# Performance work log

Hardware: AMD Instinct MI355X
Metric: run time of the kernel (lower is better)

Reference implementation:

```python
import jax, jax.numpy as jnp
import numpy as np

N, M, D_IN, D_TXT, D_OUT, H = 4096, 1024, 512, 512, 512, 8
DH = D_OUT // H


def positional_encoding(n, dim):
    # Matches PositionalEncoding: freq = exp((arange(dim//2)/dim)*ln(10000)),
    # x = pos/freq -> [L, dim//2], interleave (sin, cos) pairs -> [L, dim].
    pos = jnp.arange(n, dtype=jnp.float32)
    freq = jnp.exp((jnp.arange(dim // 2, dtype=jnp.float32) / dim) * jnp.log(jnp.float32(10000.0)))
    x = pos[:, None] / freq  # [L, dim//2]
    pe = jnp.stack((jnp.sin(x), jnp.cos(x)), axis=-1)  # [L, dim//2, 2]
    return pe.reshape(n, dim)


def setup_inputs() -> dict:
    key = jax.random.key(0)
    k1, k2, k3, k4, k5, k6 = jax.random.split(key, 6)
    s = 0.02
    return {
        "video_features": jax.random.normal(k1, (N, D_IN), dtype=jnp.float32),
        "text_features": jax.random.normal(k2, (M, D_TXT), dtype=jnp.float32),
        "Wq": jax.random.normal(k3, (H, D_IN, DH), dtype=jnp.float32) * s,
        "Wk": jax.random.normal(k4, (H, D_TXT, DH), dtype=jnp.float32) * s,
        "Wv": jax.random.normal(k5, (H, D_TXT, DH), dtype=jnp.float32) * s,
        "Wout": jax.random.normal(k6, (D_OUT, D_IN), dtype=jnp.float32) * s,
    }


def reference(video_features, text_features, Wq, Wk, Wv, Wout):
    # Batched over heads instead of the original per-head Python loop (same math).
    Q = jnp.einsum('nd,hde->hne', video_features, Wq)   # [H, N, DH]
    K = jnp.einsum('md,hde->hme', text_features, Wk)    # [H, M, DH]
    V = jnp.einsum('md,hde->hme', text_features, Wv)    # [H, M, DH]
    energies = jnp.einsum('hne,hme->hnm', Q, K)         # no scaling in original
    att = jax.nn.softmax(energies, axis=-1)             # dropout omitted (eval mode)
    y = jnp.einsum('hnm,hme->hne', att, V)              # [H, N, DH]
    y = jnp.transpose(y, (1, 0, 2)).reshape(video_features.shape[0], -1)  # concat heads
    y = y @ Wout                                        # [N, D_IN]
    y = y + positional_encoding(y.shape[0], y.shape[1])
    return y
```

## Files before the change

kernel.cpp:

```cpp
#include <hip/hip_runtime.h>
#include <hip/hip_bf16.h>
#include <math.h>

#define N_TOK 4096
#define M_TOK 1024
#define DMODEL 512
#define NHEAD 8
#define DHEAD 64
#define LOG2E 1.44269504f

typedef __attribute__((ext_vector_type(8))) short short8;
typedef __attribute__((ext_vector_type(4))) float f32x4;
typedef __attribute__((ext_vector_type(4))) float float4v;

static __device__ __forceinline__ short f2bf(float f) {
    union { float f; unsigned u; } v; v.f = f;
    unsigned r = v.u + 0x7fffu + ((v.u >> 16) & 1u);
    return (short)(r >> 16);
}

__global__ __launch_bounds__(256) void pack_kernel(
        const float* __restrict__ xv, const float* __restrict__ xt,
        const float* __restrict__ wq, const float* __restrict__ wk,
        const float* __restrict__ wv, const float* __restrict__ wo,
        short* __restrict__ xvb, short* __restrict__ xtb,
        short* __restrict__ wqb, short* __restrict__ wkb,
        short* __restrict__ wvb, short* __restrict__ wob) {
    int bid = blockIdx.x;
    int t = threadIdx.x;
    if (bid < 256) {
        __shared__ float lds[64][65];
        const float* src;
        short* dst;
        int srstride;
        int dr0, dc0;
        if (bid < 192) {
            int mat = bid >> 6;
            int hb = bid & 63;
            int h = hb >> 3, dt = hb & 7;
            const float* W = (mat == 0) ? wq : (mat == 1) ? wk : wv;
            src = W + (size_t)h * (DMODEL * DHEAD) + (size_t)(dt * 64) * DHEAD;
            srstride = DHEAD;
            dst = (mat == 0) ? wqb : (mat == 1) ? wkb : wvb;
            dr0 = h * 64;
            dc0 = dt * 64;
        } else {
            int b = bid - 192;
            int rt = b >> 3, ct = b & 7;
            src = wo + (size_t)(rt * 64) * DMODEL + ct * 64;
            srstride = DMODEL;
            dst = wob;
            dr0 = ct * 64;
            dc0 = rt * 64;
        }
        {
            int r = t >> 2, c0 = (t & 3) * 16;
            const float* s = src + (size_t)r * srstride + c0;
            #pragma unroll
            for (int j = 0; j < 4; j++) {
                float4v v = *(const float4v*)(s + j * 4);
                lds[r][c0 + j * 4 + 0] = v[0];
                lds[r][c0 + j * 4 + 1] = v[1];
                lds[r][c0 + j * 4 + 2] = v[2];
                lds[r][c0 + j * 4 + 3] = v[3];
            }
        }
        __syncthreads();
        {
            int outr = t >> 2, c0 = (t & 3) * 16;
            short8 o0, o1;
            #pragma unroll
            for (int j = 0; j < 8; j++) {
                o0[j] = f2bf(lds[c0 + j][outr]);
                o1[j] = f2bf(lds[c0 + 8 + j][outr]);
            }
            short* d = dst + (size_t)(dr0 + outr) * DMODEL + dc0 + c0;
            *(short8*)d = o0;
            *(short8*)(d + 8) = o1;
        }
        return;
    }
    int idx = (bid - 256) * 256 + t;
    int stride = (gridDim.x - 256) * 256;
    const int CXV = N_TOK * DMODEL / 8;
    const int CXT = M_TOK * DMODEL / 8;
    for (int c = idx; c < CXV; c += stride) {
        float4v f0 = *(const float4v*)&xv[c * 8];
        float4v f1 = *(const float4v*)&xv[c * 8 + 4];
        short8 o;
        #pragma unroll
        for (int j = 0; j < 4; j++) { o[j] = f2bf(f0[j]); o[j + 4] = f2bf(f1[j]); }
        *(short8*)&xvb[c * 8] = o;
    }
    for (int c = idx; c < CXT; c += stride) {
        float4v f0 = *(const float4v*)&xt[c * 8];
        float4v f1 = *(const float4v*)&xt[c * 8 + 4];
        short8 o;
        #pragma unroll
        for (int j = 0; j < 4; j++) { o[j] = f2bf(f0[j]); o[j + 4] = f2bf(f1[j]); }
        *(short8*)&xtb[c * 8] = o;
    }
}

template<typename EPI>
static __device__ __forceinline__ void gemm_body8(const short* __restrict__ A,
                                                  const short* __restrict__ BT,
                                                  int m0, int n0, EPI epi) {
    __shared__ __align__(16) short As[64][72];
    __shared__ __align__(16) short Bs[64][72];
    int t = threadIdx.x;
    int lane = t & 63, w = t >> 6;
    int wr = w & 3, wc = w >> 2;
    int l15 = lane & 15, g = lane >> 4;

    int row = t >> 3, c0 = (t & 7) * 8;
    const short* gA = A + (size_t)(m0 + row) * DMODEL + c0;
    const short* gB = BT + (size_t)(n0 + row) * DMODEL + c0;

    short8 ra = *(const short8*)gA;
    short8 rb = *(const short8*)gB;

    f32x4 acc[2] = {};
    #pragma unroll
    for (int step = 0; step < DMODEL / 64; ++step) {
        *(short8*)&As[row][c0] = ra;
        *(short8*)&Bs[row][c0] = rb;
        __syncthreads();
        if (step < DMODEL / 64 - 1) {
            gA += 64; gB += 64;
            ra = *(const short8*)gA;
            rb = *(const short8*)gB;
        }
        #pragma unroll
        for (int ks = 0; ks < 2; ks++) {
            short8 a = *(short8*)&As[wr * 16 + l15][ks * 32 + g * 8];
            #pragma unroll
            for (int fc = 0; fc < 2; fc++) {
                short8 b = *(short8*)&Bs[wc * 32 + fc * 16 + l15][ks * 32 + g * 8];
                acc[fc] = __builtin_amdgcn_mfma_f32_16x16x32_bf16(a, b, acc[fc], 0, 0, 0);
            }
        }
        __syncthreads();
    }
    #pragma unroll
    for (int fc = 0; fc < 2; fc++)
        #pragma unroll
        for (int r = 0; r < 4; r++) {
            int orow = m0 + wr * 16 + g * 4 + r;
            int ocol = n0 + wc * 32 + fc * 16 + l15;
            epi(orow, ocol, acc[fc][r]);
        }
}

__global__ __launch_bounds__(512) void gemmKV(const short* __restrict__ xtb,
                                              const short* __restrict__ wkb,
                                              const short* __restrict__ wvb,
                                              short* __restrict__ kbm,
                                              short* __restrict__ vbt) {
    int bx = blockIdx.x;
    if (bx < 128) {
        gemm_body8(xtb, wkb, (bx >> 3) * 64, (bx & 7) * 64,
                   [&](int row, int col, float v) { kbm[(size_t)row * DMODEL + col] = f2bf(v * LOG2E); });
    } else {
        int b = bx - 128;
        gemm_body8(xtb, wvb, (b >> 3) * 64, (b & 7) * 64,
                   [&](int row, int col, float v) { vbt[(size_t)col * M_TOK + row] = f2bf(v); });
    }
}

__global__ __launch_bounds__(512) void gemmOut(const short* __restrict__ A,
                                               const short* __restrict__ BT,
                                               float* __restrict__ Cout) {
    __shared__ float ifreq[256];
    if (threadIdx.x < 256)
        ifreq[threadIdx.x] = __expf(-(float)threadIdx.x * (9.210340371976184f / 512.0f));
    __syncthreads();
    gemm_body8(A, BT, blockIdx.x * 64, blockIdx.y * 64,
               [&](int row, int col, float v) {
                   float x = (float)row * ifreq[col >> 1];
                   float pe = (col & 1) ? __cosf(x) : __sinf(x);
                   Cout[(size_t)row * DMODEL + col] = v + pe;
               });
}

struct GemmS {
    short As[64][72];
    short Bs[64][72];
};
struct Merge2 {
    f32x4 macc[4][2][64];
    f32x4 mrs[4][64];
};
union ProMerge { GemmS g; Merge2 m; };

__global__ __launch_bounds__(512) void attn_kernel(const short* __restrict__ xvb,
                                                   const short* __restrict__ wqb,
                                                   const short* __restrict__ Kb,
                                                   const short* __restrict__ VbT,
                                                   short* __restrict__ Yb) {
    __shared__ __align__(16) short Ks[2][64][72];
    __shared__ __align__(16) short Vt[2][64][72];
    __shared__ __align__(16) short Ps[8][16][68];
    __shared__ __align__(16) short Qs[64][68];
    __shared__ __align__(16) ProMerge pm;

    int bid = blockIdx.x;
    int h = bid & 7;
    int n0 = (bid >> 3) * 64;
    int t = threadIdx.x;
    int lane = t & 63, w = t >> 6;
    int qg = w & 3, kh = w >> 2;
    int l15 = lane & 15, g = lane >> 4;

    {
        int row = t >> 3, c0 = (t & 7) * 8;
        const short* gA = xvb + (size_t)(n0 + row) * DMODEL + c0;
        const short* gB = wqb + (size_t)(h * DHEAD + row) * DMODEL + c0;
        short8 ra = *(const short8*)gA;
        short8 rb = *(const short8*)gB;
        int wr = w & 3, wc = w >> 2;
        f32x4 qacc[2] = {};
        #pragma unroll
        for (int step = 0; step < DMODEL / 64; ++step) {
            *(short8*)&pm.g.As[row][c0] = ra;
            *(short8*)&pm.g.Bs[row][c0] = rb;
            __syncthreads();
            if (step < DMODEL / 64 - 1) {
                gA += 64; gB += 64;
                ra = *(const short8*)gA;
                rb = *(const short8*)gB;
            }
            #pragma unroll
            for (int ks = 0; ks < 2; ks++) {
                short8 a = *(short8*)&pm.g.As[wr * 16 + l15][ks * 32 + g * 8];
                #pragma unroll
                for (int fc = 0; fc < 2; fc++) {
                    short8 b = *(short8*)&pm.g.Bs[wc * 32 + fc * 16 + l15][ks * 32 + g * 8];
                    qacc[fc] = __builtin_amdgcn_mfma_f32_16x16x32_bf16(a, b, qacc[fc], 0, 0, 0);
                }
            }
            __syncthreads();
        }
        #pragma unroll
        for (int fc = 0; fc < 2; fc++)
            #pragma unroll
            for (int r = 0; r < 4; r++)
                Qs[wr * 16 + g * 4 + r][wc * 32 + fc * 16 + l15] = f2bf(qacc[fc][r]);
        __syncthreads();
    }

    short8 qa0 = *(short8*)&Qs[qg * 16 + l15][g * 8];
    short8 qa1 = *(short8*)&Qs[qg * 16 + l15][32 + g * 8];

    int sh = t >> 8;
    int tt = t & 255;
    int row = tt >> 2, c0 = (tt & 3) * 16;
    const short* gK = Kb + (size_t)(sh * 512 + row) * DMODEL + h * DHEAD + c0;
    const short* gV = VbT + (size_t)(h * DHEAD + row) * M_TOK + sh * 512 + c0;

    short8 k0 = *(const short8*)gK;
    short8 k1 = *(const short8*)(gK + 8);
    short8 v0 = *(const short8*)gV;
    short8 v1 = *(const short8*)(gV + 8);

    f32x4 acc[4] = {};
    f32x4 rsum = {};

    for (int it = 0; it < 8; ++it) {
        *(short8*)&Ks[sh][row][c0]     = k0;
        *(short8*)&Ks[sh][row][c0 + 8] = k1;
        *(short8*)&Vt[sh][row][c0]     = v0;
        *(short8*)&Vt[sh][row][c0 + 8] = v1;
        __syncthreads();
        if (it < 7) {
            gK += (size_t)64 * DMODEL;
            gV += 64;
            k0 = *(const short8*)gK;
            k1 = *(const short8*)(gK + 8);
            v0 = *(const short8*)gV;
            v1 = *(const short8*)(gV + 8);
        }
        #pragma unroll
        for (int kt = 0; kt < 4; kt++) {
            short8 kf0 = *(short8*)&Ks[kh][kt * 16 + l15][g * 8];
            short8 kf1 = *(short8*)&Ks[kh][kt * 16 + l15][32 + g * 8];
            f32x4 e = {};
            e = __builtin_amdgcn_mfma_f32_16x16x32_bf16(qa0, kf0, e, 0, 0, 0);
            e = __builtin_amdgcn_mfma_f32_16x16x32_bf16(qa1, kf1, e, 0, 0, 0);
            #pragma unroll
            for (int r = 0; r < 4; r++) {
                float p = exp2f(e[r]);
                rsum[r] += p;
                Ps[w][g * 4 + r][kt * 16 + l15] = f2bf(p);
            }
        }
        #pragma unroll
        for (int kb2 = 0; kb2 < 2; kb2++) {
            short8 pa = *(short8*)&Ps[w][l15][kb2 * 32 + g * 8];
            #pragma unroll
            for (int nt = 0; nt < 4; nt++) {
                short8 vf = *(short8*)&Vt[kh][nt * 16 + l15][kb2 * 32 + g * 8];
                acc[nt] = __builtin_amdgcn_mfma_f32_16x16x32_bf16(pa, vf, acc[nt], 0, 0, 0);
            }
        }
        __syncthreads();
    }

    if (kh == 1) {
        pm.m.macc[qg][0][lane] = acc[0];
        pm.m.macc[qg][1][lane] = acc[1];
        pm.m.mrs[qg][lane] = rsum;
    }
    __syncthreads();
    if (kh == 0) {
        acc[0] += pm.m.macc[qg][0][lane];
        acc[1] += pm.m.macc[qg][1][lane];
        rsum += pm.m.mrs[qg][lane];
    }
    __syncthreads();
    if (kh == 1) {
        pm.m.macc[qg][0][lane] = acc[2];
        pm.m.macc[qg][1][lane] = acc[3];
    }
    __syncthreads();
    if (kh == 0) {
        acc[2] += pm.m.macc[qg][0][lane];
        acc[3] += pm.m.macc[qg][1][lane];
        #pragma unroll
        for (int r = 0; r < 4; r++) {
            float s = rsum[r];
            s += __shfl_xor(s, 1);
            s += __shfl_xor(s, 2);
            s += __shfl_xor(s, 4);
            s += __shfl_xor(s, 8);
            rsum[r] = s;
        }
        #pragma unroll
        for (int nt = 0; nt < 4; nt++)
            #pragma unroll
            for (int r = 0; r < 4; r++) {
                float y = acc[nt][r] / rsum[r];
                Yb[(size_t)(n0 + qg * 16 + g * 4 + r) * DMODEL + h * DHEAD + nt * 16 + l15] = f2bf(y);
            }
    }
}

extern "C" void kernel_launch(void* const* d_in, const int* in_sizes, int n_in,
                              void* d_out, int out_size, void* d_ws, size_t ws_size,
                              hipStream_t stream) {
    const float* xv = (const float*)d_in[0];
    const float* xt = (const float*)d_in[1];
    const float* wq = (const float*)d_in[2];
    const float* wk = (const float*)d_in[3];
    const float* wv = (const float*)d_in[4];
    const float* wo = (const float*)d_in[5];

    short* xvb = (short*)d_ws;
    short* xtb = xvb + N_TOK * DMODEL;
    short* wqb = xtb + M_TOK * DMODEL;
    short* wkb = wqb + DMODEL * DMODEL;
    short* wvb = wkb + DMODEL * DMODEL;
    short* wob = wvb + DMODEL * DMODEL;
    short* kbm = wob + DMODEL * DMODEL;
    short* vbt = kbm + M_TOK * DMODEL;
    short* yb  = vbt + M_TOK * DMODEL;

    pack_kernel<<<1280, 256, 0, stream>>>(xv, xt, wq, wk, wv, wo,
                                          xvb, xtb, wqb, wkb, wvb, wob);
    gemmKV<<<256, 512, 0, stream>>>(xtb, wkb, wvb, kbm, vbt);
    attn_kernel<<<512, 512, 0, stream>>>(xvb, wqb, kbm, vbt, yb);
    gemmOut<<<dim3(64, 8), 512, 0, stream>>>(yb, wob, (float*)d_out);
}
```

Measured before the change: 51.58 us.

## Overlay attention shared buffers, widen Q-projection K-step, prefetch K/V early

Shared memory in the attention kernel is rearranged into two unions: the Q-projection staging buffers share space with the K/V tiles, and Qs, Ps and the merge scratch share a second region. This shrinks the per-block LDS footprint so more blocks can reside per CU. The Q projection now stages 128-wide K chunks, halving its loop trips and barriers, and the first K/V tile loads are issued before the projection so their latency overlaps with it. An extra barrier is added after reading Qs so Ps can safely reuse that space, and the K/V row padding changes from 72 to 68, which may alter LDS bank conflicts.

```diff
diff --git a/kernel.cpp b/kernel.cpp
--- a/kernel.cpp
+++ b/kernel.cpp
@@ -183,26 +183,21 @@
                });
 }
 
-struct GemmS {
-    short As[64][72];
-    short Bs[64][72];
-};
-struct Merge2 {
-    f32x4 macc[4][2][64];
-    f32x4 mrs[4][64];
-};
-union ProMerge { GemmS g; Merge2 m; };
+struct ProKV { short As[64][136]; short Bs[64][136]; };
+struct KVS   { short Ks[2][64][68]; short Vt[2][64][68]; };
+union Reg1 { ProKV p; KVS kv; };
+struct QsS   { short Qs[64][68]; };
+struct PsS   { short Ps[8][16][68]; };
+struct Merge2 { f32x4 macc[4][2][64]; f32x4 mrs[4][64]; };
+union Reg2 { QsS q; PsS ps; Merge2 m; };
 
 __global__ __launch_bounds__(512) void attn_kernel(const short* __restrict__ xvb,
                                                    const short* __restrict__ wqb,
                                                    const short* __restrict__ Kb,
                                                    const short* __restrict__ VbT,
                                                    short* __restrict__ Yb) {
-    __shared__ __align__(16) short Ks[2][64][72];
-    __shared__ __align__(16) short Vt[2][64][72];
-    __shared__ __align__(16) short Ps[8][16][68];
-    __shared__ __align__(16) short Qs[64][68];
-    __shared__ __align__(16) ProMerge pm;
+    __shared__ __align__(16) Reg1 r1;
+    __shared__ __align__(16) Reg2 r2;
 
     int bid = blockIdx.x;
     int h = bid & 7;
@@ -212,65 +207,71 @@
     int qg = w & 3, kh = w >> 2;
     int l15 = lane & 15, g = lane >> 4;
 
-    {
-        int row = t >> 3, c0 = (t & 7) * 8;
-        const short* gA = xvb + (size_t)(n0 + row) * DMODEL + c0;
-        const short* gB = wqb + (size_t)(h * DHEAD + row) * DMODEL + c0;
-        short8 ra = *(const short8*)gA;
-        short8 rb = *(const short8*)gB;
-        int wr = w & 3, wc = w >> 2;
-        f32x4 qacc[2] = {};
-        #pragma unroll
-        for (int step = 0; step < DMODEL / 64; ++step) {
-            *(short8*)&pm.g.As[row][c0] = ra;
-            *(short8*)&pm.g.Bs[row][c0] = rb;
-            __syncthreads();
-            if (step < DMODEL / 64 - 1) {
-                gA += 64; gB += 64;
-                ra = *(const short8*)gA;
-                rb = *(const short8*)gB;
-            }
-            #pragma unroll
-            for (int ks = 0; ks < 2; ks++) {
-                short8 a = *(short8*)&pm.g.As[wr * 16 + l15][ks * 32 + g * 8];
-                #pragma unroll
-                for (int fc = 0; fc < 2; fc++) {
-                    short8 b = *(short8*)&pm.g.Bs[wc * 32 + fc * 16 + l15][ks * 32 + g * 8];
-                    qacc[fc] = __builtin_amdgcn_mfma_f32_16x16x32_bf16(a, b, qacc[fc], 0, 0, 0);
-                }
-            }
-            __syncthreads();
-        }
-        #pragma unroll
-        for (int fc = 0; fc < 2; fc++)
-            #pragma unroll
-            for (int r = 0; r < 4; r++)
-                Qs[wr * 16 + g * 4 + r][wc * 32 + fc * 16 + l15] = f2bf(qacc[fc][r]);
-        __syncthreads();
-    }
-
-    short8 qa0 = *(short8*)&Qs[qg * 16 + l15][g * 8];
-    short8 qa1 = *(short8*)&Qs[qg * 16 + l15][32 + g * 8];
-
     int sh = t >> 8;
     int tt = t & 255;
-    int row = tt >> 2, c0 = (tt & 3) * 16;
-    const short* gK = Kb + (size_t)(sh * 512 + row) * DMODEL + h * DHEAD + c0;
-    const short* gV = VbT + (size_t)(h * DHEAD + row) * M_TOK + sh * 512 + c0;
-
+    int srow = tt >> 2, sc0 = (tt & 3) * 16;
+    const short* gK = Kb + (size_t)(sh * 512 + srow) * DMODEL + h * DHEAD + sc0;
+    const short* gV = VbT + (size_t)(h * DHEAD + srow) * M_TOK + sh * 512 + sc0;
     short8 k0 = *(const short8*)gK;
     short8 k1 = *(const short8*)(gK + 8);
     short8 v0 = *(const short8*)gV;
     short8 v1 = *(const short8*)(gV + 8);
 
+    {
+        int row = t >> 3, c0 = (t & 7) * 16;
+        const short* gA = xvb + (size_t)(n0 + row) * DMODEL + c0;
+        const short* gB = wqb + (size_t)(h * DHEAD + row) * DMODEL + c0;
+        short8 ra0 = *(const short8*)gA;
+        short8 ra1 = *(const short8*)(gA + 8);
+        short8 rb0 = *(const short8*)gB;
+        short8 rb1 = *(const short8*)(gB + 8);
+        int wr = w & 3, wc = w >> 2;
+        f32x4 qacc[2] = {};
+        #pragma unroll
+        for (int step = 0; step < 4; ++step) {
+            *(short8*)&r1.p.As[row][c0]     = ra0;
+            *(short8*)&r1.p.As[row][c0 + 8] = ra1;
+            *(short8*)&r1.p.Bs[row][c0]     = rb0;
+            *(short8*)&r1.p.Bs[row][c0 + 8] = rb1;
+            __syncthreads();
+            if (step < 3) {
+                gA += 128; gB += 128;
+                ra0 = *(const short8*)gA;
+                ra1 = *(const short8*)(gA + 8);
+                rb0 = *(const short8*)gB;
+                rb1 = *(const short8*)(gB + 8);
+            }
+            #pragma unroll
+            for (int ks = 0; ks < 4; ks++) {
+                short8 a = *(short8*)&r1.p.As[wr * 16 + l15][ks * 32 + g * 8];
+                #pragma unroll
+                for (int fc = 0; fc < 2; fc++) {
+                    short8 b = *(short8*)&r1.p.Bs[wc * 32 + fc * 16 + l15][ks * 32 + g * 8];
+                    qacc[fc] = __builtin_amdgcn_mfma_f32_16x16x32_bf16(a, b, qacc[fc], 0, 0, 0);
+                }
+            }
+            __syncthreads();
+        }
+        #pragma unroll
+        for (int fc = 0; fc < 2; fc++)
+            #pragma unroll
+            for (int r = 0; r < 4; r++)
+                r2.q.Qs[wr * 16 + g * 4 + r][wc * 32 + fc * 16 + l15] = f2bf(qacc[fc][r]);
+        __syncthreads();
+    }
+
+    short8 qa0 = *(short8*)&r2.q.Qs[qg * 16 + l15][g * 8];
+    short8 qa1 = *(short8*)&r2.q.Qs[qg * 16 + l15][32 + g * 8];
+    __syncthreads();
+
     f32x4 acc[4] = {};
     f32x4 rsum = {};
 
     for (int it = 0; it < 8; ++it) {
-        *(short8*)&Ks[sh][row][c0]     = k0;
-        *(short8*)&Ks[sh][row][c0 + 8] = k1;
-        *(short8*)&Vt[sh][row][c0]     = v0;
-        *(short8*)&Vt[sh][row][c0 + 8] = v1;
+        *(short8*)&r1.kv.Ks[sh][srow][sc0]     = k0;
+        *(short8*)&r1.kv.Ks[sh][srow][sc0 + 8] = k1;
+        *(short8*)&r1.kv.Vt[sh][srow][sc0]     = v0;
+        *(short8*)&r1.kv.Vt[sh][srow][sc0 + 8] = v1;
         __syncthreads();
         if (it < 7) {
             gK += (size_t)64 * DMODEL;
@@ -282,8 +283,8 @@
         }
         #pragma unroll
         for (int kt = 0; kt < 4; kt++) {
-            short8 kf0 = *(short8*)&Ks[kh][kt * 16 + l15][g * 8];
-            short8 kf1 = *(short8*)&Ks[kh][kt * 16 + l15][32 + g * 8];
+            short8 kf0 = *(short8*)&r1.kv.Ks[kh][kt * 16 + l15][g * 8];
+            short8 kf1 = *(short8*)&r1.kv.Ks[kh][kt * 16 + l15][32 + g * 8];
             f32x4 e = {};
             e = __builtin_amdgcn_mfma_f32_16x16x32_bf16(qa0, kf0, e, 0, 0, 0);
             e = __builtin_amdgcn_mfma_f32_16x16x32_bf16(qa1, kf1, e, 0, 0, 0);
@@ -291,15 +292,15 @@
             for (int r = 0; r < 4; r++) {
                 float p = exp2f(e[r]);
                 rsum[r] += p;
-                Ps[w][g * 4 + r][kt * 16 + l15] = f2bf(p);
+                r2.ps.Ps[w][g * 4 + r][kt * 16 + l15] = f2bf(p);
             }
         }
         #pragma unroll
         for (int kb2 = 0; kb2 < 2; kb2++) {
-            short8 pa = *(short8*)&Ps[w][l15][kb2 * 32 + g * 8];
+            short8 pa = *(short8*)&r2.ps.Ps[w][l15][kb2 * 32 + g * 8];
             #pragma unroll
             for (int nt = 0; nt < 4; nt++) {
-                short8 vf = *(short8*)&Vt[kh][nt * 16 + l15][kb2 * 32 + g * 8];
+                short8 vf = *(short8*)&r1.kv.Vt[kh][nt * 16 + l15][kb2 * 32 + g * 8];
                 acc[nt] = __builtin_amdgcn_mfma_f32_16x16x32_bf16(pa, vf, acc[nt], 0, 0, 0);
             }
         }
@@ -307,25 +308,25 @@
     }
 
     if (kh == 1) {
-        pm.m.macc[qg][0][lane] = acc[0];
-        pm.m.macc[qg][1][lane] = acc[1];
-        pm.m.mrs[qg][lane] = rsum;
+        r2.m.macc[qg][0][lane] = acc[0];
+        r2.m.macc[qg][1][lane] = acc[1];
+        r2.m.mrs[qg][lane] = rsum;
     }
     __syncthreads();
     if (kh == 0) {
-        acc[0] += pm.m.macc[qg][0][lane];
-        acc[1] += pm.m.macc[qg][1][lane];
-        rsum += pm.m.mrs[qg][lane];
+        acc[0] += r2.m.macc[qg][0][lane];
+        acc[1] += r2.m.macc[qg][1][lane];
+        rsum += r2.m.mrs[qg][lane];
     }
     __syncthreads();
     if (kh == 1) {
-        pm.m.macc[qg][0][lane] = acc[2];
-        pm.m.macc[qg][1][lane] = acc[3];
+        r2.m.macc[qg][0][lane] = acc[2];
+        r2.m.macc[qg][1][lane] = acc[3];
     }
     __syncthreads();
     if (kh == 0) {
-        acc[2] += pm.m.macc[qg][0][lane];
-        acc[3] += pm.m.macc[qg][1][lane];
+        acc[2] += r2.m.macc[qg][0][lane];
+        acc[3] += r2.m.macc[qg][1][lane];
         #pragma unroll
         for (int r = 0; r < 4; r++) {
             float s = rsum[r];
```

Result: slower. 52.96 us (+2.7%).
